# Optimization experiments

Hardware: AMD Instinct MI355X
Metric: run time of the kernel (lower is better)

## Reference

```python
import jax, jax.numpy as jnp
import numpy as np

N, E, G = 20000, 320000, 256
FXD, FXT, OD = 78, 954, 128


def _lin(key, fan_in, fan_out, scale=0.05):
    return jax.random.normal(key, (fan_in, fan_out), dtype=jnp.float32) * scale


def setup_inputs() -> dict:
    key = jax.random.key(0)
    ks = jax.random.split(key, 24)
    inp = {
        "x1": jax.random.normal(ks[0], (N, FXD), dtype=jnp.float32),
        "edge_index1": jax.random.randint(ks[1], (2, E), 0, N, dtype=jnp.int32),
        "batch1": (jnp.arange(N, dtype=jnp.int32) * G) // N,  # sorted, every graph non-empty
        "x2": jax.random.normal(ks[2], (N, FXD), dtype=jnp.float32),
        "edge_index2": jax.random.randint(ks[3], (2, E), 0, N, dtype=jnp.int32),
        "batch2": (jnp.arange(N, dtype=jnp.int32) * G) // N,
        "cell": jax.random.normal(ks[4], (G, FXT), dtype=jnp.float32),
        # GCNConv weights (shared across the two drug branches, as in the module)
        "Wc1": _lin(ks[5], FXD, FXD), "bc1": jnp.zeros((FXD,), jnp.float32),
        "Wc2": _lin(ks[6], FXD, FXD * 2), "bc2": jnp.zeros((FXD * 2,), jnp.float32),
        "Wc3": _lin(ks[7], FXD * 2, FXD * 4), "bc3": jnp.zeros((FXD * 4,), jnp.float32),
        "Wg1": _lin(ks[8], FXD * 4, FXD * 2), "bg1": jnp.zeros((FXD * 2,), jnp.float32),
        "Wg2": _lin(ks[9], FXD * 2, OD), "bg2": jnp.zeros((OD,), jnp.float32),
        # cell reduction MLP 954 -> 2048 -> 512 -> 256
        "Wr1": _lin(ks[10], FXT, 2048), "br1": jnp.zeros((2048,), jnp.float32),
        "Wr2": _lin(ks[11], 2048, 512), "br2": jnp.zeros((512,), jnp.float32),
        "Wr3": _lin(ks[12], 512, OD * 2), "br3": jnp.zeros((OD * 2,), jnp.float32),
        # head MLP 512 -> 1024 -> 512 -> 128 -> 2
        "Wf1": _lin(ks[13], OD * 4, 1024), "bf1": jnp.zeros((1024,), jnp.float32),
        "Wf2": _lin(ks[14], 1024, 512), "bf2": jnp.zeros((512,), jnp.float32),
        "Wf3": _lin(ks[15], 512, 128), "bf3": jnp.zeros((128,), jnp.float32),
        "Wo": _lin(ks[16], 128, 2), "bo": jnp.zeros((2,), jnp.float32),
    }
    return inp


def gcn_conv(x, W, b, src, dst, n):
    """PyG GCNConv: h = D^{-1/2}(A+I)D^{-1/2} (x W) + b (self-loops added)."""
    h = x @ W
    loops = jnp.arange(n, dtype=src.dtype)
    s = jnp.concatenate([src, loops])
    d = jnp.concatenate([dst, loops])
    deg = jax.ops.segment_sum(jnp.ones_like(s, dtype=h.dtype), d, num_segments=n)
    dinv = jax.lax.rsqrt(deg)  # deg >= 1 due to self-loops
    norm = dinv[s] * dinv[d]  # [E+N]
    out = jax.ops.segment_sum(h[s] * norm[:, None], d, num_segments=n)
    return out + b


def drug_branch(x, ei, batch, Wc1, bc1, Wc2, bc2, Wc3, bc3, Wg1, bg1, Wg2, bg2):
    src, dst = ei[0], ei[1]
    n = x.shape[0]
    x = jax.nn.relu(gcn_conv(x, Wc1, bc1, src, dst, n))
    x = jax.nn.relu(gcn_conv(x, Wc2, bc2, src, dst, n))
    x = jax.nn.relu(gcn_conv(x, Wc3, bc3, src, dst, n))
    x = jax.ops.segment_max(x, batch, num_segments=G)  # global max pool -> [G, 312]
    x = jax.nn.relu(x @ Wg1 + bg1)
    x = x @ Wg2 + bg2  # dropout is identity in eval mode
    return x


def reference(x1, edge_index1, batch1, x2, edge_index2, batch2, cell,
              Wc1, bc1, Wc2, bc2, Wc3, bc3, Wg1, bg1, Wg2, bg2,
              Wr1, br1, Wr2, br2, Wr3, br3,
              Wf1, bf1, Wf2, bf2, Wf3, bf3, Wo, bo):
    g1 = drug_branch(x1, edge_index1, batch1, Wc1, bc1, Wc2, bc2, Wc3, bc3, Wg1, bg1, Wg2, bg2)
    g2 = drug_branch(x2, edge_index2, batch2, Wc1, bc1, Wc2, bc2, Wc3, bc3, Wg1, bg1, Wg2, bg2)
    # F.normalize(cell, p=2, dim=1)
    cv = cell / jnp.maximum(jnp.linalg.norm(cell, axis=1, keepdims=True), 1e-12)
    cv = jax.nn.relu(cv @ Wr1 + br1)
    cv = jax.nn.relu(cv @ Wr2 + br2)
    cv = jax.nn.relu(cv @ Wr3 + br3)
    xc = jnp.concatenate([g1, g2, cv], axis=1)  # [G, 512]
    xc = jax.nn.relu(xc @ Wf1 + bf1)
    xc = jax.nn.relu(xc @ Wf2 + bf2)
    xc = jax.nn.relu(xc @ Wf3 + bf3)
    return xc @ Wo + bo  # [G, 2]
```

## Files before the change

### kernel.cpp

```cpp
#include <hip/hip_runtime.h>

#define N_NODES 20000
#define N_EDGES 320000
#define N_GRAPH 256
#define ECHUNK 2048
#define DCAP 64

__device__ __forceinline__ ushort f2b(float f) {
  unsigned u = __float_as_uint(f);
  u += 0x7FFFu + ((u >> 16) & 1u);
  return (ushort)(u >> 16);
}
__device__ __forceinline__ float b2f(ushort u) {
  return __uint_as_float(((unsigned)u) << 16);
}

typedef __attribute__((ext_vector_type(8))) short bf16x8;
typedef __attribute__((ext_vector_type(4))) float f32x4;

template <int POOL>
__launch_bounds__(256)
__global__ void gemm_mfma(const ushort* __restrict__ A, int lda,
                          const ushort* __restrict__ Bt, int ldbt,
                          void* __restrict__ Cv, int ldc,
                          const float* __restrict__ bias,
                          int Nr, int Kpad, int M, int do_relu, int obf,
                          const float* __restrict__ dsc, int cwz,
                          const int* __restrict__ bA, const int* __restrict__ bB,
                          int nsplit, int gA, int gB, int gTot) {
  constexpr int BM = 128, BN = 128, BK = 32, LK = 40;
  __shared__ __align__(16) ushort Asl[BM][LK];
  __shared__ __align__(16) ushort Bsl[BN][LK];
  const int tid = threadIdx.x;
  const int Cc = (M + BN - 1) / BN;
  const int R = (Nr + BM - 1) / BM;
  const int RR = (R + 7) >> 3;
  const int xz = blockIdx.x & 7, g = blockIdx.x >> 3;
  const int q = g / Cc;
  const int by = xz * RR + q, bx = g - q * Cc;
  if (by >= R) return;
  const int row0 = by * BM, col0 = bx * BN;

  const int lane = tid & 63, w = tid >> 6;
  const int a_r = tid >> 1, a_h = tid & 1;

  const int nst = Kpad / BK;

  uint4 pa0, pa1, pb0, pb1;
  auto load_tile = [&](int k0) {
    if (row0 + a_r < Nr) {
      const uint4* p = (const uint4*)(A + (size_t)(row0 + a_r) * lda + k0 + a_h * 16);
      pa0 = p[0]; pa1 = p[1];
    } else {
      pa0 = make_uint4(0u, 0u, 0u, 0u); pa1 = pa0;
    }
    const uint4* pq = (const uint4*)(Bt + (size_t)(col0 + a_r) * ldbt + k0 + a_h * 16);
    pb0 = pq[0]; pb1 = pq[1];
  };
  auto commit = [&]() {
    *(uint4*)&Asl[a_r][a_h * 16] = pa0;
    *(uint4*)&Asl[a_r][a_h * 16 + 8] = pa1;
    *(uint4*)&Bsl[a_r][a_h * 16] = pb0;
    *(uint4*)&Bsl[a_r][a_h * 16 + 8] = pb1;
  };

  f32x4 acc[2][8] = {};
  const int mrow = w * 32;
  const int lm = lane & 15, lq = (lane >> 4) * 8;

  load_tile(0);
  for (int t = 0; t < nst; ++t) {
    commit();
    __syncthreads();
    if (t + 1 < nst) load_tile((t + 1) * BK);
    bf16x8 af0 = *(const bf16x8*)&Asl[mrow + lm][lq];
    bf16x8 af1 = *(const bf16x8*)&Asl[mrow + 16 + lm][lq];
#pragma unroll
    for (int nt = 0; nt < 8; ++nt) {
      bf16x8 bf = *(const bf16x8*)&Bsl[nt * 16 + lm][lq];
      acc[0][nt] = __builtin_amdgcn_mfma_f32_16x16x32_bf16(af0, bf, acc[0][nt], 0, 0, 0);
      acc[1][nt] = __builtin_amdgcn_mfma_f32_16x16x32_bf16(af1, bf, acc[1][nt], 0, 0, 0);
    }
    __syncthreads();
  }

  const int rquad = (lane >> 4) * 4;

  if constexpr (POOL) {
    __shared__ int Ps[4][BN];
    for (int idx = tid; idx < 4 * BN; idx += 256) Ps[idx >> 7][idx & 127] = 0;
    __syncthreads();
    const int g0 = (row0 < nsplit) ? gA + bA[row0] : gB + bB[row0 - nsplit];
    int gr8[2][4];
#pragma unroll
    for (int mt = 0; mt < 2; ++mt)
#pragma unroll
      for (int r = 0; r < 4; ++r) {
        const int rr = row0 + mrow + mt * 16 + rquad + r;
        gr8[mt][r] = (rr < Nr)
                         ? ((rr < nsplit) ? gA + bA[rr] : gB + bB[rr - nsplit])
                         : -1;
      }
#pragma unroll
    for (int mt = 0; mt < 2; ++mt)
#pragma unroll
      for (int nt = 0; nt < 8; ++nt) {
        const int cl = nt * 16 + lm;
        if (col0 + cl >= M) continue;
        const float bv = bias[col0 + cl];
#pragma unroll
        for (int r = 0; r < 4; ++r) {
          const int gg = gr8[mt][r];
          if (gg < 0) continue;
          const float v = fmaxf(acc[mt][nt][r] + bv, 0.f);
          atomicMax(&Ps[gg - g0][cl], __float_as_int(v));
        }
      }
    __syncthreads();
    for (int idx = tid; idx < 4 * BN; idx += 256) {
      const int s = idx >> 7, c = idx & 127;
      const int gg = g0 + s, cc = col0 + c;
      if (gg < gTot && cc < M)
        atomicMax((int*)Cv + (size_t)gg * ldc + cc, Ps[s][c]);
    }
    return;
  }

  const int cz = (cwz > M) ? cwz : M;
#pragma unroll
  for (int mt = 0; mt < 2; ++mt) {
#pragma unroll
    for (int nt = 0; nt < 8; ++nt) {
      const int cc = col0 + nt * 16 + lm;
      if (cc >= cz) continue;
      const bool cval = cc < M;
      const float bv = (cval && bias) ? bias[cc] : 0.f;
#pragma unroll
      for (int r = 0; r < 4; ++r) {
        const int rr = row0 + mrow + mt * 16 + rquad + r;
        if (rr >= Nr) continue;
        float v = cval ? (acc[mt][nt][r] + bv) : 0.f;
        if (do_relu) v = fmaxf(v, 0.f);
        if (dsc) v *= dsc[rr];
        if (obf) ((ushort*)Cv)[(size_t)rr * ldc + cc] = f2b(v);
        else     ((float*)Cv)[(size_t)rr * ldc + cc] = v;
      }
    }
  }
}

struct GJob {
  const void* A; const ushort* Bt; void* C; const float* bias;
  int lda, a_f32, ldbt, ldc, Nr, Kpad, M, relu, obf, rsplit, cpad, rb, cb, blk0;
};

__launch_bounds__(256)
__global__ void gemm_grp(GJob j0, GJob j1, int njobs) {
  GJob j = (njobs > 1 && (int)blockIdx.x >= j1.blk0) ? j1 : j0;
  const int local = blockIdx.x - j.blk0;
  const int by = local / j.cb, bx = local - by * j.cb;
  const int row0 = by * 32, col0 = bx * 64;
  const int tid = threadIdx.x, lane = tid & 63, w = tid >> 6;

  __shared__ __align__(16) char smem[32768];
  ushort (*Asl)[32][40] = (ushort (*)[32][40])smem;
  ushort (*Bsl)[64][40] = (ushort (*)[64][40])(smem + 10240);
  float  (*Rs)[32][64]  = (float  (*)[32][64])smem;

  const int a_r = lane >> 1, a_h = lane & 1;
  const int lm = lane & 15, lq = (lane >> 4) * 8;
  const int nst = j.Kpad / 32;

  uint4 ra[4], rb[4];
  auto gload = [&](int t) {
    const int k0 = t * 32;
    const int ar = row0 + a_r;
    if (j.a_f32) {
      if (ar < j.Nr) {
        const uint4* p = (const uint4*)((const float*)j.A + (size_t)ar * j.lda + k0 + a_h * 16);
        ra[0] = p[0]; ra[1] = p[1]; ra[2] = p[2]; ra[3] = p[3];
      } else {
        ra[0] = make_uint4(0u, 0u, 0u, 0u); ra[1] = ra[0]; ra[2] = ra[0]; ra[3] = ra[0];
      }
    } else {
      if (ar < j.Nr) {
        const uint4* p = (const uint4*)((const ushort*)j.A + (size_t)ar * j.lda + k0 + a_h * 16);
        ra[0] = p[0]; ra[1] = p[1];
      } else {
        ra[0] = make_uint4(0u, 0u, 0u, 0u); ra[1] = ra[0];
      }
    }
    const uint4* q = (const uint4*)(j.Bt + (size_t)(col0 + lane) * j.ldbt + k0);
    rb[0] = q[0]; rb[1] = q[1]; rb[2] = q[2]; rb[3] = q[3];
  };
  auto commit = [&]() {
    if (j.a_f32) {
      ushort tmp[16];
      const float* f = (const float*)&ra[0];
#pragma unroll
      for (int q2 = 0; q2 < 16; ++q2) tmp[q2] = f2b(f[q2]);
      *(uint4*)&Asl[w][a_r][a_h * 16]     = *(uint4*)&tmp[0];
      *(uint4*)&Asl[w][a_r][a_h * 16 + 8] = *(uint4*)&tmp[8];
    } else {
      *(uint4*)&Asl[w][a_r][a_h * 16]     = ra[0];
      *(uint4*)&Asl[w][a_r][a_h * 16 + 8] = ra[1];
    }
    *(uint4*)&Bsl[w][lane][0]  = rb[0];
    *(uint4*)&Bsl[w][lane][8]  = rb[1];
    *(uint4*)&Bsl[w][lane][16] = rb[2];
    *(uint4*)&Bsl[w][lane][24] = rb[3];
  };

  f32x4 acc[2][4] = {};
  if (w < nst) {
    gload(w);
    for (int t = w; t < nst; t += 4) {
      commit();
      bf16x8 af0 = *(const bf16x8*)&Asl[w][lm][lq];
      bf16x8 af1 = *(const bf16x8*)&Asl[w][16 + lm][lq];
      bf16x8 bq0 = *(const bf16x8*)&Bsl[w][lm][lq];
      bf16x8 bq1 = *(const bf16x8*)&Bsl[w][16 + lm][lq];
      bf16x8 bq2 = *(const bf16x8*)&Bsl[w][32 + lm][lq];
      bf16x8 bq3 = *(const bf16x8*)&Bsl[w][48 + lm][lq];
      if (t + 4 < nst) gload(t + 4);
      acc[0][0] = __builtin_amdgcn_mfma_f32_16x16x32_bf16(af0, bq0, acc[0][0], 0, 0, 0);
      acc[0][1] = __builtin_amdgcn_mfma_f32_16x16x32_bf16(af0, bq1, acc[0][1], 0, 0, 0);
      acc[0][2] = __builtin_amdgcn_mfma_f32_16x16x32_bf16(af0, bq2, acc[0][2], 0, 0, 0);
      acc[0][3] = __builtin_amdgcn_mfma_f32_16x16x32_bf16(af0, bq3, acc[0][3], 0, 0, 0);
      acc[1][0] = __builtin_amdgcn_mfma_f32_16x16x32_bf16(af1, bq0, acc[1][0], 0, 0, 0);
      acc[1][1] = __builtin_amdgcn_mfma_f32_16x16x32_bf16(af1, bq1, acc[1][1], 0, 0, 0);
      acc[1][2] = __builtin_amdgcn_mfma_f32_16x16x32_bf16(af1, bq2, acc[1][2], 0, 0, 0);
      acc[1][3] = __builtin_amdgcn_mfma_f32_16x16x32_bf16(af1, bq3, acc[1][3], 0, 0, 0);
    }
  }

  __syncthreads();
  const int rquad = (lane >> 4) * 4;
#pragma unroll
  for (int mt = 0; mt < 2; ++mt)
#pragma unroll
    for (int nt = 0; nt < 4; ++nt)
#pragma unroll
      for (int r = 0; r < 4; ++r)
        Rs[w][mt * 16 + rquad + r][nt * 16 + lm] = acc[mt][nt][r];
  __syncthreads();

  const int rrow = tid >> 3, cs = (tid & 7) * 8;
  float v[8];
  {
    float4 x0 = *(const float4*)&Rs[0][rrow][cs];
    float4 x1 = *(const float4*)&Rs[0][rrow][cs + 4];
    v[0] = x0.x; v[1] = x0.y; v[2] = x0.z; v[3] = x0.w;
    v[4] = x1.x; v[5] = x1.y; v[6] = x1.z; v[7] = x1.w;
  }
#pragma unroll
  for (int ww = 1; ww < 4; ++ww) {
    float4 x0 = *(const float4*)&Rs[ww][rrow][cs];
    float4 x1 = *(const float4*)&Rs[ww][rrow][cs + 4];
    v[0] += x0.x; v[1] += x0.y; v[2] += x0.z; v[3] += x0.w;
    v[4] += x1.x; v[5] += x1.y; v[6] += x1.z; v[7] += x1.w;
  }
  const int rg = row0 + rrow;
  if (rg < j.Nr) {
    int rm = rg, rq = 0;
    if (j.rsplit) { rq = rg / j.rsplit; rm = rg - rq * j.rsplit; }
#pragma unroll
    for (int q = 0; q < 8; ++q) {
      const int cc = col0 + cs + q;
      if (cc >= j.cpad) break;
      float x = 0.f;
      if (cc < j.M) {
        x = v[q] + j.bias[cc];
        if (j.relu) x = fmaxf(x, 0.f);
      }
      const size_t di = (size_t)rm * j.ldc + (size_t)rq * j.M + cc;
      if (j.obf) ((ushort*)j.C)[di] = f2b(x);
      else       ((float*)j.C)[di] = x;
    }
  }
}

struct WJob { const float* W; ushort* T; int Mv, Kv, Mp, Kp, blk0; };
struct WArgs { WJob j[11]; int wblocks; const float* cell; ushort* cv; };

__launch_bounds__(256)
__global__ void prep_all(WArgs a) {
  const int bid = blockIdx.x, tid = threadIdx.x;
  if (bid < a.wblocks) {
    __shared__ float t[32][33];
    int ji = 0;
#pragma unroll
    for (int i = 1; i < 11; ++i)
      if (bid >= a.j[i].blk0) ji = i;
    WJob wj = a.j[ji];
    const int lt = bid - wj.blk0;
    const int ktiles = wj.Kp >> 5;
    const int tn = lt / ktiles, tk = lt - tn * ktiles;
    const int n0 = tn << 5, k0 = tk << 5;
    const int c = tid & 31, r = tid >> 5;
    const int nn = n0 + c;
#pragma unroll
    for (int i = 0; i < 4; ++i) {
      const int k = k0 + r + i * 8;
      t[r + i * 8][c] = (k < wj.Kv && nn < wj.Mv) ? wj.W[(size_t)k * wj.Mv + nn] : 0.f;
    }
    __syncthreads();
    const int k = k0 + c;
#pragma unroll
    for (int i = 0; i < 4; ++i) {
      const int n = n0 + r + i * 8;
      wj.T[(size_t)n * wj.Kp + k] = f2b(t[c][r + i * 8]);
    }
    return;
  }
  __shared__ float red[256];
  const int g = bid - a.wblocks;
  const float* row = a.cell + (size_t)g * 954;
  float s = 0.f;
  for (int f = tid; f < 954; f += 256) { float vv = row[f]; s += vv * vv; }
  red[tid] = s;
  __syncthreads();
  for (int off2 = 128; off2 > 0; off2 >>= 1) {
    if (tid < off2) red[tid] += red[tid + off2];
    __syncthreads();
  }
  const float inv = 1.f / fmaxf(sqrtf(red[0]), 1e-12f);
  ushort* orow = a.cv + (size_t)g * 960;
  for (int f = tid; f < 954; f += 256) orow[f] = f2b(row[f] * inv);
  for (int f = 954 + tid; f < 960; f += 256) orow[f] = 0;
}

template<int BM, int BN, int TM, int TN>
__launch_bounds__(256)
__global__ void gemm_t(const float* __restrict__ A, int lda,
                       const float* __restrict__ B, int ldb,
                       float* __restrict__ C, int ldc, int zstride,
                       const float* __restrict__ bias,
                       int Nr, int K, int M, int do_relu, int kchunk) {
  constexpr int BK = 16;
  constexpr int LDA = BM + 4;
  __shared__ __align__(16) float As[BK][LDA];
  __shared__ __align__(16) float Bs[BK][BN];
  const int tid = threadIdx.x;
  const int row0 = blockIdx.y * BM, col0 = blockIdx.x * BN;
  constexpr int NX = BN / TN;
  const int tx = tid % NX, ty = tid / NX;
  float acc[TM][TN] = {};
  const int klo = blockIdx.z * kchunk;
  const int khi = min(klo + kchunk, K);

  constexpr int AIT = BM * BK / 4 / 256;
  constexpr int BIT = BK * BN / 4 / 256;
  float4 pa[AIT], pb[BIT];

  auto load_tile = [&](int k0) {
#pragma unroll
    for (int it = 0; it < AIT; ++it) {
      const int s = it * 256 + tid;
      const int row = s >> 2, kq = (s & 3) << 2;
      float4 av = make_float4(0.f, 0.f, 0.f, 0.f);
      const int gr = row0 + row, gk = k0 + kq;
      if (gr < Nr) {
        const float* Ap = A + (size_t)gr * lda + gk;
        if (gk + 3 < khi) { av.x = Ap[0]; av.y = Ap[1]; av.z = Ap[2]; av.w = Ap[3]; }
        else {
          if (gk     < khi) av.x = Ap[0];
          if (gk + 1 < khi) av.y = Ap[1];
          if (gk + 2 < khi) av.z = Ap[2];
        }
      }
      pa[it] = av;
    }
#pragma unroll
    for (int it = 0; it < BIT; ++it) {
      const int s = it * 256 + tid;
      const int kr = s / (BN / 4), c = (s % (BN / 4)) << 2;
      float4 bv = make_float4(0.f, 0.f, 0.f, 0.f);
      const int gk = k0 + kr, gc = col0 + c;
      if (gk < khi) {
        const float* Bp = B + (size_t)gk * ldb + gc;
        if (gc + 3 < M) { bv.x = Bp[0]; bv.y = Bp[1]; bv.z = Bp[2]; bv.w = Bp[3]; }
        else {
          if (gc     < M) bv.x = Bp[0];
          if (gc + 1 < M) bv.y = Bp[1];
          if (gc + 2 < M) bv.z = Bp[2];
        }
      }
      pb[it] = bv;
    }
  };

  load_tile(klo);
  for (int k0 = klo; k0 < khi; k0 += BK) {
#pragma unroll
    for (int it = 0; it < AIT; ++it) {
      const int s = it * 256 + tid;
      const int row = s >> 2, kq = (s & 3) << 2;
      As[kq    ][row] = pa[it].x;
      As[kq + 1][row] = pa[it].y;
      As[kq + 2][row] = pa[it].z;
      As[kq + 3][row] = pa[it].w;
    }
#pragma unroll
    for (int it = 0; it < BIT; ++it) {
      const int s = it * 256 + tid;
      const int kr = s / (BN / 4), c = (s % (BN / 4)) << 2;
      *(float4*)&Bs[kr][c] = pb[it];
    }
    __syncthreads();
    if (k0 + BK < khi) load_tile(k0 + BK);
#pragma unroll
    for (int kk = 0; kk < BK; ++kk) {
      float ar[TM], br[TN];
#pragma unroll
      for (int i = 0; i < TM; i += 4)
        *(float4*)&ar[i] = *(const float4*)&As[kk][ty * TM + i];
      if constexpr (TN == 8) {
        *(float4*)&br[0] = *(const float4*)&Bs[kk][tx * 4];
        *(float4*)&br[4] = *(const float4*)&Bs[kk][BN / 2 + tx * 4];
      } else {
        *(float4*)&br[0] = *(const float4*)&Bs[kk][tx * TN];
      }
#pragma unroll
      for (int i = 0; i < TM; ++i)
#pragma unroll
        for (int j = 0; j < TN; ++j)
          acc[i][j] += ar[i] * br[j];
    }
    __syncthreads();
  }

  float* Cz = C + (size_t)blockIdx.z * zstride;
#pragma unroll
  for (int i = 0; i < TM; ++i) {
    const int r = row0 + ty * TM + i;
    if (r >= Nr) continue;
    float* Crow = Cz + (size_t)r * ldc;
#pragma unroll
    for (int g = 0; g < TN / 4; ++g) {
      const int c = col0 + (TN == 8 ? g * (BN / 2) : 0) + tx * 4;
      if (c + 3 < M) {
        float4 v;
        v.x = acc[i][g * 4 + 0]; v.y = acc[i][g * 4 + 1];
        v.z = acc[i][g * 4 + 2]; v.w = acc[i][g * 4 + 3];
        if (bias) { v.x += bias[c]; v.y += bias[c + 1]; v.z += bias[c + 2]; v.w += bias[c + 3]; }
        if (do_relu) {
          v.x = fmaxf(v.x, 0.f); v.y = fmaxf(v.y, 0.f);
          v.z = fmaxf(v.z, 0.f); v.w = fmaxf(v.w, 0.f);
        }
        *(float4*)&Crow[c] = v;
      } else {
#pragma unroll
        for (int j = 0; j < 4; ++j) {
          if (c + j >= M) continue;
          float v = acc[i][g * 4 + j];
          if (bias) v += bias[c + j];
          if (do_relu) v = fmaxf(v, 0.f);
          Crow[c + j] = v;
        }
      }
    }
  }
}

__global__ void scatterb_kernel(const int* __restrict__ e1, const int* __restrict__ e2,
                                int* __restrict__ cnt, ushort* __restrict__ col_idx,
                                int E, int npass, int rng) {
  const int xcd = blockIdx.x & 7;
  const int lo = xcd * rng, hi = lo + rng;
  const int base = (blockIdx.x >> 3) * ECHUNK;
  const int TE = npass * E;
  for (int i = threadIdx.x; i < ECHUNK; i += 256) {
    int e = base + i;
    if (e >= TE) break;
    int d, s;
    if (e < E) { d = e1[E + e]; s = e1[e]; }
    else { int jj = e - E; d = N_NODES + e2[E + jj]; s = N_NODES + e2[jj]; }
    if (d >= lo && d < hi) {
      int p = atomicAdd(&cnt[d], 1);
      if (p < DCAP) col_idx[((size_t)d << 6) + p] = (ushort)s;
    }
  }
}

__global__ void dinv_cvt_kernel(const int* __restrict__ cnt, float* __restrict__ dinv,
                                const float* __restrict__ xa, const float* __restrict__ xb,
                                int nsplit, ushort* __restrict__ dst, int total) {
  int gid = blockIdx.x * blockDim.x + threadIdx.x;
  if (gid >= total) return;
  int n = gid / 10, v = gid - n * 10;
  const float sc = rsqrtf((float)(cnt[n] + 1));
  if (v == 0) dinv[n] = sc;
  const float* src = (n < nsplit) ? xa + (size_t)n * 78 : xb + (size_t)(n - nsplit) * 78;
  const int f0 = v * 8;
  ushort o[8];
#pragma unroll
  for (int jj = 0; jj < 8; ++jj)
    o[jj] = (f0 + jj < 78) ? f2b(src[f0 + jj] * sc) : 0;
  ((uint4*)(dst + (size_t)n * 80))[v] = *(uint4*)o;
}

__device__ __forceinline__ void acc8(float* a, uint4 u) {
  a[0] += __uint_as_float(u.x << 16);
  a[1] += __uint_as_float(u.x & 0xFFFF0000u);
  a[2] += __uint_as_float(u.y << 16);
  a[3] += __uint_as_float(u.y & 0xFFFF0000u);
  a[4] += __uint_as_float(u.z << 16);
  a[5] += __uint_as_float(u.z & 0xFFFF0000u);
  a[6] += __uint_as_float(u.w << 16);
  a[7] += __uint_as_float(u.w & 0xFFFF0000u);
}

__global__ void aggb_flat(const ushort* __restrict__ h, const int* __restrict__ cnt,
                          const ushort* __restrict__ col_idx, const float* __restrict__ dinv,
                          ushort* __restrict__ out, int in_ld, int out_ld,
                          int V, int total) {
  int gid = blockIdx.x * blockDim.x + threadIdx.x;
  if (gid >= total) return;
  int n = gid / V, v = gid - n * V;
  const uint4* hv = (const uint4*)h;
  const int ivs = in_ld >> 3;
  float a[8] = {};
  acc8(a, hv[(size_t)n * ivs + v]);
  const int beg = n << 6;
  const int end = beg + min(cnt[n], DCAP);
  int e = beg;
  for (; e + 3 < end; e += 4) {
    int s0 = col_idx[e], s1 = col_idx[e + 1], s2 = col_idx[e + 2], s3 = col_idx[e + 3];
    uint4 u0 = hv[(size_t)s0 * ivs + v], u1 = hv[(size_t)s1 * ivs + v];
    uint4 u2 = hv[(size_t)s2 * ivs + v], u3 = hv[(size_t)s3 * ivs + v];
    acc8(a, u0); acc8(a, u1); acc8(a, u2); acc8(a, u3);
  }
  for (; e < end; ++e)
    acc8(a, hv[(size_t)col_idx[e] * ivs + v]);
  const float din = dinv[n];
  ushort o[8];
#pragma unroll
  for (int jj = 0; jj < 8; ++jj) o[jj] = f2b(din * a[jj]);
  ((uint4*)(out + (size_t)n * out_ld))[v] = *(uint4*)o;
}

extern "C" void kernel_launch(void* const* d_in, const int* in_sizes, int n_in,
                              void* d_out, int out_size, void* d_ws, size_t ws_size,
                              hipStream_t stream) {
  (void)in_sizes; (void)n_in; (void)out_size;
  const float* x1  = (const float*)d_in[0];
  const int*   ei1 = (const int*)d_in[1];
  const int*   bt1 = (const int*)d_in[2];
  const float* x2  = (const float*)d_in[3];
  const int*   ei2 = (const int*)d_in[4];
  const int*   bt2 = (const int*)d_in[5];
  const float* cell = (const float*)d_in[6];
  const float* Wc1 = (const float*)d_in[7];  const float* bc1 = (const float*)d_in[8];
  const float* Wc2 = (const float*)d_in[9];  const float* bc2 = (const float*)d_in[10];
  const float* Wc3 = (const float*)d_in[11]; const float* bc3 = (const float*)d_in[12];
  const float* Wg1 = (const float*)d_in[13]; const float* bg1 = (const float*)d_in[14];
  const float* Wg2 = (const float*)d_in[15]; const float* bg2 = (const float*)d_in[16];
  const float* Wr1 = (const float*)d_in[17]; const float* br1 = (const float*)d_in[18];
  const float* Wr2 = (const float*)d_in[19]; const float* br2 = (const float*)d_in[20];
  const float* Wr3 = (const float*)d_in[21]; const float* br3 = (const float*)d_in[22];
  const float* Wf1 = (const float*)d_in[23]; const float* bf1 = (const float*)d_in[24];
  const float* Wf2 = (const float*)d_in[25]; const float* bf2 = (const float*)d_in[26];
  const float* Wf3 = (const float*)d_in[27]; const float* bf3 = (const float*)d_in[28];
  const float* Wo  = (const float*)d_in[29]; const float* bo  = (const float*)d_in[30];
  float* out = (float*)d_out;

  const bool batched = ws_size >= (size_t)95 * 1024 * 1024;
  const int NPASS = batched ? 2 : 1;
  const int NN = NPASS * N_NODES;

  char* ws = (char*)d_ws;
  size_t off = 0;
  auto alloc_f = [&](size_t ne) {
    ne = (ne + 3) & ~(size_t)3;
    float* p = (float*)(ws + off); off += ne * 4; return p;
  };
  auto alloc_i = [&](size_t ne) {
    ne = (ne + 3) & ~(size_t)3;
    int* p = (int*)(ws + off); off += ne * 4; return p;
  };
  ushort* xb16w = (ushort*)alloc_f((size_t)NN * 80);
  ushort* ab16  = (ushort*)alloc_f((size_t)NN * 80);
  ushort* xb16s = (ushort*)alloc_f((size_t)NN * 40);
  float* dinv   = alloc_f(NN);
  int* cnt      = alloc_i(NN);
  float* pooled = alloc_f((size_t)512 * 320);
  ushort* cv16  = (ushort*)alloc_f((size_t)N_GRAPH * 480);
  ushort* wg1o  = (ushort*)alloc_f((size_t)512 * 80);
  ushort* wr1o  = (ushort*)alloc_f((size_t)256 * 1024);
  ushort* wr2o  = (ushort*)alloc_f((size_t)256 * 256);
  ushort* catbuf = (ushort*)alloc_f((size_t)256 * 256);
  ushort* wf1o  = (ushort*)alloc_f((size_t)256 * 512);
  ushort* wf2o  = (ushort*)alloc_f((size_t)256 * 256);
  float* wf3o   = alloc_f((size_t)256 * 128);
  ushort* wc1t  = (ushort*)alloc_f(128 * 96 / 2);
  ushort* wc2t  = (ushort*)alloc_f(256 * 96 / 2);
  ushort* wc3t  = (ushort*)alloc_f(384 * 160 / 2);
  ushort* wr1t  = (ushort*)alloc_f(2048 * 960 / 2);
  ushort* wr2t  = (ushort*)alloc_f(512 * 2048 / 2);
  ushort* wf1t  = (ushort*)alloc_f(1024 * 512 / 2);
  ushort* wg1t  = (ushort*)alloc_f(192 * 320 / 2);
  ushort* wg2t  = (ushort*)alloc_f(128 * 160 / 2);
  ushort* wr3t  = (ushort*)alloc_f(256 * 512 / 2);
  ushort* wf2t  = (ushort*)alloc_f(512 * 1024 / 2);
  ushort* wf3t  = (ushort*)alloc_f(128 * 512 / 2);
  ushort* col_idx = (ushort*)alloc_i((size_t)NN * DCAP / 2);

  auto gemm_small = [&](const float* A, int lda, const float* B, int ldb, float* C, int ldc,
                        const float* bias, int Nr, int K, int M, int relu) {
    dim3 grid((M + 63) / 64, (Nr + 63) / 64, 1);
    gemm_t<64, 64, 4, 4><<<grid, 256, 0, stream>>>(A, lda, B, ldb, C, ldc, 0, bias,
                                                   Nr, K, M, relu, K);
  };
  auto mfma = [&](const ushort* A, int lda, const ushort* Bt, int ldbt, void* C, int ldc,
                  const float* bias, int Nr, int Kpad, int M, int relu, int obf,
                  const float* dsc, int cwz) {
    int Cc = (M + 127) / 128, R = (Nr + 127) / 128, RR = (R + 7) >> 3;
    dim3 grid(8 * RR * Cc, 1, 1);
    gemm_mfma<0><<<grid, 256, 0, stream>>>(A, lda, Bt, ldbt, C, ldc, bias, Nr, Kpad, M,
                                           relu, obf, dsc, cwz,
                                           nullptr, nullptr, 0, 0, 0, 0);
  };
  auto mfma_pool = [&](const ushort* A, int lda, const ushort* Bt, int ldbt,
                       const float* bias, int Nr, int Kpad, int M,
                       const int* bA, const int* bB, int nsplit, int gA, int gB, int gTot) {
    int Cc = (M + 127) / 128, R = (Nr + 127) / 128, RR = (R + 7) >> 3;
    dim3 grid(8 * RR * Cc, 1, 1);
    gemm_mfma<1><<<grid, 256, 0, stream>>>(A, lda, Bt, ldbt, pooled, 320, bias,
                                           Nr, Kpad, M, 1, 0, nullptr, 0,
                                           bA, bB, nsplit, gA, gB, gTot);
  };
  auto mkjob = [&](const void* A, int lda, int a_f32, const ushort* Bt, int ldbt,
                   void* C, int ldc, const float* bias, int Nr, int Kpad, int M,
                   int relu, int obf, int rsplit, int cpad) {
    GJob g; g.A = A; g.Bt = Bt; g.C = C; g.bias = bias;
    g.lda = lda; g.a_f32 = a_f32; g.ldbt = ldbt; g.ldc = ldc;
    g.Nr = Nr; g.Kpad = Kpad; g.M = M; g.relu = relu; g.obf = obf;
    g.rsplit = rsplit; g.cpad = cpad;
    g.rb = (Nr + 31) / 32; g.cb = (M + 63) / 64; g.blk0 = 0;
    return g;
  };
  auto grp1 = [&](GJob a) {
    gemm_grp<<<a.rb * a.cb, 256, 0, stream>>>(a, a, 1);
  };
  auto grp2 = [&](GJob a, GJob b) {
    b.blk0 = a.rb * a.cb;
    gemm_grp<<<b.blk0 + b.rb * b.cb, 256, 0, stream>>>(a, b, 2);
  };

  {
    WArgs wa{};
    int nj = 0, wb = 0;
    auto addw = [&](const float* W, ushort* T, int Mv, int Kv, int Mp, int Kp) {
      wa.j[nj].W = W; wa.j[nj].T = T; wa.j[nj].Mv = Mv; wa.j[nj].Kv = Kv;
      wa.j[nj].Mp = Mp; wa.j[nj].Kp = Kp; wa.j[nj].blk0 = wb;
      wb += (Mp >> 5) * (Kp >> 5); ++nj;
    };
    addw(Wc1, wc1t,   78,   78,  128,   96);
    addw(Wc2, wc2t,  156,   78,  256,   96);
    addw(Wc3, wc3t,  312,  156,  384,  160);
    addw(Wr1, wr1t, 2048,  954, 2048,  960);
    addw(Wr2, wr2t,  512, 2048,  512, 2048);
    addw(Wf1, wf1t, 1024,  512, 1024,  512);
    addw(Wg1, wg1t,  156,  312,  192,  320);
    addw(Wg2, wg2t,  128,  156,  128,  160);
    addw(Wr3, wr3t,  256,  512,  256,  512);
    addw(Wf2, wf2t,  512, 1024,  512, 1024);
    addw(Wf3, wf3t,  128,  512,  128,  512);
    wa.wblocks = wb; wa.cell = cell; wa.cv = cv16;
    prep_all<<<wb + N_GRAPH, 256, 0, stream>>>(wa);
  }

  auto drug_pass = [&](const float* xa, const float* xb, const int* eia, const int* eib,
                       const int* bta, const int* btb, int npass, int pool_base,
                       int zero_pool) {
    const int nn = npass * N_NODES;
    const int te = npass * N_EDGES;
    const int rng = nn / 8;
    const int echunks = (te + ECHUNK - 1) / ECHUNK;
    hipMemsetAsync(cnt, 0, (size_t)nn * 4 + (zero_pool ? (size_t)512 * 320 * 4 : 0),
                   stream);
    scatterb_kernel<<<8 * echunks, 256, 0, stream>>>(eia, eib, cnt, col_idx,
                                                     N_EDGES, npass, rng);
    {
      int tot = nn * 10;
      dinv_cvt_kernel<<<(tot + 255) / 256, 256, 0, stream>>>(
          cnt, dinv, xa, xb, (npass == 2) ? N_NODES : nn, xb16s, tot);
    }
    {
      int tot = nn * 10;
      aggb_flat<<<(tot + 255) / 256, 256, 0, stream>>>(xb16s, cnt, col_idx, dinv,
                                                       ab16, 80, 96, 10, tot);
    }
    mfma(ab16, 96, wc1t, 96, xb16s, 80, bc1, nn, 96, 78, 1, 1, dinv, 80);
    {
      int tot = nn * 10;
      aggb_flat<<<(tot + 255) / 256, 256, 0, stream>>>(xb16s, cnt, col_idx, dinv,
                                                       ab16, 80, 96, 10, tot);
    }
    mfma(ab16, 96, wc2t, 96, xb16w, 160, bc2, nn, 96, 156, 1, 1, dinv, 160);
    {
      int tot = nn * 20;
      aggb_flat<<<(tot + 255) / 256, 256, 0, stream>>>(xb16w, cnt, col_idx, dinv,
                                                       ab16, 160, 160, 20, tot);
    }
    mfma_pool(ab16, 160, wc3t, 160, bc3, nn, 160, 312,
              bta, btb, (npass == 2) ? N_NODES : nn,
              pool_base, pool_base + N_GRAPH, pool_base + npass * N_GRAPH);
  };

  if (batched) {
    drug_pass(x1, x2, ei1, ei2, bt1, bt2, 2, 0, 1);
  } else {
    drug_pass(x1, x1, ei1, ei1, bt1, bt1, 1, 0, 1);
    drug_pass(x2, x2, ei2, ei2, bt2, bt2, 1, N_GRAPH, 0);
  }

  grp2(mkjob(pooled, 320, 1, wg1t, 320, wg1o, 160, bg1, 512, 320, 156, 1, 1, 0, 160),
       mkjob(cv16,   960, 0, wr1t, 960, wr1o, 2048, br1, 256, 960, 2048, 1, 1, 0, 2048));
  grp2(mkjob(wg1o,  160, 0, wg2t,  160, catbuf, 512, bg2, 512,  160,  128, 0, 1, 256, 128),
       mkjob(wr1o, 2048, 0, wr2t, 2048, wr2o,   512, br2, 256, 2048,  512, 1, 1, 0, 512));
  grp1(mkjob(wr2o, 512, 0, wr3t, 512, catbuf + 256, 512, br3, 256, 512, 256, 1, 1, 0, 256));
  grp1(mkjob(catbuf, 512, 0, wf1t,  512, wf1o, 1024, bf1, 256,  512, 1024, 1, 1, 0, 1024));
  grp1(mkjob(wf1o,  1024, 0, wf2t, 1024, wf2o,  512, bf2, 256, 1024,  512, 1, 1, 0, 512));
  grp1(mkjob(wf2o,   512, 0, wf3t,  512, wf3o,  128, bf3, 256,  512,  128, 1, 0, 0, 128));
  gemm_small(wf3o, 128, Wo, 2, out, 2, bo, N_GRAPH, 128, 2, 0);
}
```

Measured before the change: 398.6 us.

## Fuse GCN aggregation into MFMA GEMM and merge edge scatter into prep kernel

Adds a gemm_fused kernel that performs the neighbour aggregation for layers 1 and 2 straight into shared memory and then runs the bf16 MFMA GEMM with bias, ReLU and dinv scaling. This removes two separate aggregation kernels and the round-trip of the aggregated matrix through global memory. The edge scatter is folded into the prep_all launch in the batched path, and the final 128x2 GEMM becomes a tiny dedicated kernel, all to cut launch count. In exchange, the fused kernel redoes the gather per 64-row tile, has lower MFMA tile occupancy, and adds a non-batched path with separate memsets.

```diff
diff --git a/kernel.cpp b/kernel.cpp
--- a/kernel.cpp
+++ b/kernel.cpp
@@ -17,6 +17,107 @@
 
 typedef __attribute__((ext_vector_type(8))) short bf16x8;
 typedef __attribute__((ext_vector_type(4))) float f32x4;
+
+__device__ __forceinline__ void acc8(float* a, uint4 u) {
+  a[0] += __uint_as_float(u.x << 16);
+  a[1] += __uint_as_float(u.x & 0xFFFF0000u);
+  a[2] += __uint_as_float(u.y << 16);
+  a[3] += __uint_as_float(u.y & 0xFFFF0000u);
+  a[4] += __uint_as_float(u.z << 16);
+  a[5] += __uint_as_float(u.z & 0xFFFF0000u);
+  a[6] += __uint_as_float(u.w << 16);
+  a[7] += __uint_as_float(u.w & 0xFFFF0000u);
+}
+
+template <int BN_T>
+__launch_bounds__(256)
+__global__ void gemm_fused(const ushort* __restrict__ h,
+                           const int* __restrict__ cnt,
+                           const ushort* __restrict__ col_idx,
+                           const float* __restrict__ dinv,
+                           const ushort* __restrict__ Bt, int ldbt,
+                           ushort* __restrict__ C, int ldc,
+                           const float* __restrict__ bias,
+                           int Nr, int M, int cwz) {
+  constexpr int BM = 64, BN = BN_T * 16, LA = 104;
+  __shared__ __align__(16) ushort Afull[BM][LA];
+  __shared__ __align__(16) ushort Bsl[BN][40];
+  const int tid = threadIdx.x;
+  const int R = (Nr + BM - 1) / BM;
+  const int RR = (R + 7) >> 3;
+  const int xz = blockIdx.x & 7, g = blockIdx.x >> 3;
+  const int by = xz * RR + g;
+  if (by >= R) return;
+  const int row0 = by * BM;
+  const int lane = tid & 63, w = tid >> 6;
+  const uint4* hv = (const uint4*)h;
+
+  for (int task = tid; task < BM * 10; task += 256) {
+    const int r = task / 10, c = task - r * 10;
+    const int n = row0 + r;
+    uint4 val = make_uint4(0u, 0u, 0u, 0u);
+    if (n < Nr) {
+      float a[8] = {};
+      acc8(a, hv[(size_t)n * 10 + c]);
+      const int beg = n << 6;
+      const int end = beg + min(cnt[n], DCAP);
+      int e = beg;
+      for (; e + 3 < end; e += 4) {
+        int s0 = col_idx[e], s1 = col_idx[e + 1];
+        int s2 = col_idx[e + 2], s3 = col_idx[e + 3];
+        acc8(a, hv[(size_t)s0 * 10 + c]); acc8(a, hv[(size_t)s1 * 10 + c]);
+        acc8(a, hv[(size_t)s2 * 10 + c]); acc8(a, hv[(size_t)s3 * 10 + c]);
+      }
+      for (; e < end; ++e) acc8(a, hv[(size_t)col_idx[e] * 10 + c]);
+      const float dn = dinv[n];
+      ushort o[8];
+#pragma unroll
+      for (int j = 0; j < 8; ++j) o[j] = f2b(dn * a[j]);
+      val = *(uint4*)o;
+    }
+    *(uint4*)&Afull[r][c * 8] = val;
+  }
+  for (int task = tid; task < BM * 2; task += 256) {
+    const int r = task >> 1, c2 = task & 1;
+    *(uint4*)&Afull[r][80 + c2 * 8] = make_uint4(0u, 0u, 0u, 0u);
+  }
+  __syncthreads();
+
+  f32x4 acc[BN_T] = {};
+  const int mrow = w * 16;
+  const int lm = lane & 15, lq = (lane >> 4) * 8;
+  for (int t = 0; t < 3; ++t) {
+    const int k0 = t * 32;
+    for (int s = tid; s < BN * 4; s += 256) {
+      const int br = s >> 2, bo = (s & 3) * 8;
+      *(uint4*)&Bsl[br][bo] = *(const uint4*)&Bt[(size_t)br * ldbt + k0 + bo];
+    }
+    __syncthreads();
+    bf16x8 af = *(const bf16x8*)&Afull[mrow + lm][k0 + lq];
+#pragma unroll
+    for (int nt = 0; nt < BN_T; ++nt) {
+      bf16x8 bf = *(const bf16x8*)&Bsl[nt * 16 + lm][lq];
+      acc[nt] = __builtin_amdgcn_mfma_f32_16x16x32_bf16(af, bf, acc[nt], 0, 0, 0);
+    }
+    __syncthreads();
+  }
+
+  const int rquad = (lane >> 4) * 4;
+#pragma unroll
+  for (int nt = 0; nt < BN_T; ++nt) {
+    const int cc = nt * 16 + lm;
+    if (cc >= cwz) continue;
+    const bool cval = cc < M;
+    const float bv = cval ? bias[cc] : 0.f;
+#pragma unroll
+    for (int r = 0; r < 4; ++r) {
+      const int rr = row0 + mrow + rquad + r;
+      if (rr >= Nr) continue;
+      float v = cval ? fmaxf(acc[nt][r] + bv, 0.f) * dinv[rr] : 0.f;
+      C[(size_t)rr * ldc + cc] = f2b(v);
+    }
+  }
+}
 
 template <int POOL>
 __launch_bounds__(256)
@@ -281,7 +382,10 @@
 }
 
 struct WJob { const float* W; ushort* T; int Mv, Kv, Mp, Kp, blk0; };
-struct WArgs { WJob j[11]; int wblocks; const float* cell; ushort* cv; };
+struct WArgs {
+  WJob j[11]; int wblocks; const float* cell; ushort* cv;
+  const int* e1; const int* e2; int* cnt; ushort* col; int E, npass, rng, scatB;
+};
 
 __launch_bounds__(256)
 __global__ void prep_all(WArgs a) {
@@ -313,152 +417,38 @@
     }
     return;
   }
-  __shared__ float red[256];
-  const int g = bid - a.wblocks;
-  const float* row = a.cell + (size_t)g * 954;
-  float s = 0.f;
-  for (int f = tid; f < 954; f += 256) { float vv = row[f]; s += vv * vv; }
-  red[tid] = s;
-  __syncthreads();
-  for (int off2 = 128; off2 > 0; off2 >>= 1) {
-    if (tid < off2) red[tid] += red[tid + off2];
+  if (bid < a.wblocks + N_GRAPH) {
+    __shared__ float red[256];
+    const int g = bid - a.wblocks;
+    const float* row = a.cell + (size_t)g * 954;
+    float s = 0.f;
+    for (int f = tid; f < 954; f += 256) { float vv = row[f]; s += vv * vv; }
+    red[tid] = s;
     __syncthreads();
-  }
-  const float inv = 1.f / fmaxf(sqrtf(red[0]), 1e-12f);
-  ushort* orow = a.cv + (size_t)g * 960;
-  for (int f = tid; f < 954; f += 256) orow[f] = f2b(row[f] * inv);
-  for (int f = 954 + tid; f < 960; f += 256) orow[f] = 0;
-}
-
-template<int BM, int BN, int TM, int TN>
-__launch_bounds__(256)
-__global__ void gemm_t(const float* __restrict__ A, int lda,
-                       const float* __restrict__ B, int ldb,
-                       float* __restrict__ C, int ldc, int zstride,
-                       const float* __restrict__ bias,
-                       int Nr, int K, int M, int do_relu, int kchunk) {
-  constexpr int BK = 16;
-  constexpr int LDA = BM + 4;
-  __shared__ __align__(16) float As[BK][LDA];
-  __shared__ __align__(16) float Bs[BK][BN];
-  const int tid = threadIdx.x;
-  const int row0 = blockIdx.y * BM, col0 = blockIdx.x * BN;
-  constexpr int NX = BN / TN;
-  const int tx = tid % NX, ty = tid / NX;
-  float acc[TM][TN] = {};
-  const int klo = blockIdx.z * kchunk;
-  const int khi = min(klo + kchunk, K);
-
-  constexpr int AIT = BM * BK / 4 / 256;
-  constexpr int BIT = BK * BN / 4 / 256;
-  float4 pa[AIT], pb[BIT];
-
-  auto load_tile = [&](int k0) {
-#pragma unroll
-    for (int it = 0; it < AIT; ++it) {
-      const int s = it * 256 + tid;
-      const int row = s >> 2, kq = (s & 3) << 2;
-      float4 av = make_float4(0.f, 0.f, 0.f, 0.f);
-      const int gr = row0 + row, gk = k0 + kq;
-      if (gr < Nr) {
-        const float* Ap = A + (size_t)gr * lda + gk;
-        if (gk + 3 < khi) { av.x = Ap[0]; av.y = Ap[1]; av.z = Ap[2]; av.w = Ap[3]; }
-        else {
-          if (gk     < khi) av.x = Ap[0];
-          if (gk + 1 < khi) av.y = Ap[1];
-          if (gk + 2 < khi) av.z = Ap[2];
-        }
-      }
-      pa[it] = av;
-    }
-#pragma unroll
-    for (int it = 0; it < BIT; ++it) {
-      const int s = it * 256 + tid;
-      const int kr = s / (BN / 4), c = (s % (BN / 4)) << 2;
-      float4 bv = make_float4(0.f, 0.f, 0.f, 0.f);
-      const int gk = k0 + kr, gc = col0 + c;
-      if (gk < khi) {
-        const float* Bp = B + (size_t)gk * ldb + gc;
-        if (gc + 3 < M) { bv.x = Bp[0]; bv.y = Bp[1]; bv.z = Bp[2]; bv.w = Bp[3]; }
-        else {
-          if (gc     < M) bv.x = Bp[0];
-          if (gc + 1 < M) bv.y = Bp[1];
-          if (gc + 2 < M) bv.z = Bp[2];
-        }
-      }
-      pb[it] = bv;
-    }
-  };
-
-  load_tile(klo);
-  for (int k0 = klo; k0 < khi; k0 += BK) {
-#pragma unroll
-    for (int it = 0; it < AIT; ++it) {
-      const int s = it * 256 + tid;
-      const int row = s >> 2, kq = (s & 3) << 2;
-      As[kq    ][row] = pa[it].x;
-      As[kq + 1][row] = pa[it].y;
-      As[kq + 2][row] = pa[it].z;
-      As[kq + 3][row] = pa[it].w;
-    }
-#pragma unroll
-    for (int it = 0; it < BIT; ++it) {
-      const int s = it * 256 + tid;
-      const int kr = s / (BN / 4), c = (s % (BN / 4)) << 2;
-      *(float4*)&Bs[kr][c] = pb[it];
-    }
-    __syncthreads();
-    if (k0 + BK < khi) load_tile(k0 + BK);
-#pragma unroll
-    for (int kk = 0; kk < BK; ++kk) {
-      float ar[TM], br[TN];
-#pragma unroll
-      for (int i = 0; i < TM; i += 4)
-        *(float4*)&ar[i] = *(const float4*)&As[kk][ty * TM + i];
-      if constexpr (TN == 8) {
-        *(float4*)&br[0] = *(const float4*)&Bs[kk][tx * 4];
-        *(float4*)&br[4] = *(const float4*)&Bs[kk][BN / 2 + tx * 4];
-      } else {
-        *(float4*)&br[0] = *(const float4*)&Bs[kk][tx * TN];
-      }
-#pragma unroll
-      for (int i = 0; i < TM; ++i)
-#pragma unroll
-        for (int j = 0; j < TN; ++j)
-          acc[i][j] += ar[i] * br[j];
-    }
-    __syncthreads();
-  }
-
-  float* Cz = C + (size_t)blockIdx.z * zstride;
-#pragma unroll
-  for (int i = 0; i < TM; ++i) {
-    const int r = row0 + ty * TM + i;
-    if (r >= Nr) continue;
-    float* Crow = Cz + (size_t)r * ldc;
-#pragma unroll
-    for (int g = 0; g < TN / 4; ++g) {
-      const int c = col0 + (TN == 8 ? g * (BN / 2) : 0) + tx * 4;
-      if (c + 3 < M) {
-        float4 v;
-        v.x = acc[i][g * 4 + 0]; v.y = acc[i][g * 4 + 1];
-        v.z = acc[i][g * 4 + 2]; v.w = acc[i][g * 4 + 3];
-        if (bias) { v.x += bias[c]; v.y += bias[c + 1]; v.z += bias[c + 2]; v.w += bias[c + 3]; }
-        if (do_relu) {
-          v.x = fmaxf(v.x, 0.f); v.y = fmaxf(v.y, 0.f);
-          v.z = fmaxf(v.z, 0.f); v.w = fmaxf(v.w, 0.f);
-        }
-        *(float4*)&Crow[c] = v;
-      } else {
-#pragma unroll
-        for (int j = 0; j < 4; ++j) {
-          if (c + j >= M) continue;
-          float v = acc[i][g * 4 + j];
-          if (bias) v += bias[c + j];
-          if (do_relu) v = fmaxf(v, 0.f);
-          Crow[c + j] = v;
-        }
-      }
+    for (int off2 = 128; off2 > 0; off2 >>= 1) {
+      if (tid < off2) red[tid] += red[tid + off2];
+      __syncthreads();
+    }
+    const float inv = 1.f / fmaxf(sqrtf(red[0]), 1e-12f);
+    ushort* orow = a.cv + (size_t)g * 960;
+    for (int f = tid; f < 954; f += 256) orow[f] = f2b(row[f] * inv);
+    for (int f = 954 + tid; f < 960; f += 256) orow[f] = 0;
+    return;
+  }
+  const int sb = bid - a.wblocks - N_GRAPH;
+  const int xcd = sb & 7;
+  const int lo = xcd * a.rng, hi = lo + a.rng;
+  const int base = (sb >> 3) * ECHUNK;
+  const int TE = a.npass * a.E;
+  for (int i = tid; i < ECHUNK; i += 256) {
+    int e = base + i;
+    if (e >= TE) break;
+    int d, s;
+    if (e < a.E) { d = a.e1[a.E + e]; s = a.e1[e]; }
+    else { int jj = e - a.E; d = N_NODES + a.e2[a.E + jj]; s = N_NODES + a.e2[jj]; }
+    if (d >= lo && d < hi) {
+      int p = atomicAdd(&a.cnt[d], 1);
+      if (p < DCAP) a.col[((size_t)d << 6) + p] = (ushort)s;
     }
   }
 }
@@ -498,17 +488,6 @@
   for (int jj = 0; jj < 8; ++jj)
     o[jj] = (f0 + jj < 78) ? f2b(src[f0 + jj] * sc) : 0;
   ((uint4*)(dst + (size_t)n * 80))[v] = *(uint4*)o;
-}
-
-__device__ __forceinline__ void acc8(float* a, uint4 u) {
-  a[0] += __uint_as_float(u.x << 16);
-  a[1] += __uint_as_float(u.x & 0xFFFF0000u);
-  a[2] += __uint_as_float(u.y << 16);
-  a[3] += __uint_as_float(u.y & 0xFFFF0000u);
-  a[4] += __uint_as_float(u.z << 16);
-  a[5] += __uint_as_float(u.z & 0xFFFF0000u);
-  a[6] += __uint_as_float(u.w << 16);
-  a[7] += __uint_as_float(u.w & 0xFFFF0000u);
 }
 
 __global__ void aggb_flat(const ushort* __restrict__ h, const int* __restrict__ cnt,
@@ -538,6 +517,17 @@
 #pragma unroll
   for (int jj = 0; jj < 8; ++jj) o[jj] = f2b(din * a[jj]);
   ((uint4*)(out + (size_t)n * out_ld))[v] = *(uint4*)o;
+}
+
+__global__ void wo_kernel(const float* __restrict__ wf3o, const float* __restrict__ Wo,
+                          const float* __restrict__ bo, float* __restrict__ out) {
+  int gid = blockIdx.x * blockDim.x + threadIdx.x;
+  if (gid >= N_GRAPH * 2) return;
+  int row = gid >> 1, col = gid & 1;
+  float v = bo[col];
+  const float* a = wf3o + (size_t)row * 128;
+  for (int k = 0; k < 128; ++k) v += a[k] * Wo[k * 2 + col];
+  out[gid] = v;
 }
 
 extern "C" void kernel_launch(void* const* d_in, const int* in_sizes, int n_in,
@@ -594,7 +584,7 @@
   ushort* wf2o  = (ushort*)alloc_f((size_t)256 * 256);
   float* wf3o   = alloc_f((size_t)256 * 128);
   ushort* wc1t  = (ushort*)alloc_f(128 * 96 / 2);
-  ushort* wc2t  = (ushort*)alloc_f(256 * 96 / 2);
+  ushort* wc2t  = (ushort*)alloc_f(192 * 96 / 2);
   ushort* wc3t  = (ushort*)alloc_f(384 * 160 / 2);
   ushort* wr1t  = (ushort*)alloc_f(2048 * 960 / 2);
   ushort* wr2t  = (ushort*)alloc_f(512 * 2048 / 2);
@@ -606,21 +596,6 @@
   ushort* wf3t  = (ushort*)alloc_f(128 * 512 / 2);
   ushort* col_idx = (ushort*)alloc_i((size_t)NN * DCAP / 2);
 
-  auto gemm_small = [&](const float* A, int lda, const float* B, int ldb, float* C, int ldc,
-                        const float* bias, int Nr, int K, int M, int relu) {
-    dim3 grid((M + 63) / 64, (Nr + 63) / 64, 1);
-    gemm_t<64, 64, 4, 4><<<grid, 256, 0, stream>>>(A, lda, B, ldb, C, ldc, 0, bias,
-                                                   Nr, K, M, relu, K);
-  };
-  auto mfma = [&](const ushort* A, int lda, const ushort* Bt, int ldbt, void* C, int ldc,
-                  const float* bias, int Nr, int Kpad, int M, int relu, int obf,
-                  const float* dsc, int cwz) {
-    int Cc = (M + 127) / 128, R = (Nr + 127) / 128, RR = (R + 7) >> 3;
-    dim3 grid(8 * RR * Cc, 1, 1);
-    gemm_mfma<0><<<grid, 256, 0, stream>>>(A, lda, Bt, ldbt, C, ldc, bias, Nr, Kpad, M,
-                                           relu, obf, dsc, cwz,
-                                           nullptr, nullptr, 0, 0, 0, 0);
-  };
   auto mfma_pool = [&](const ushort* A, int lda, const ushort* Bt, int ldbt,
                        const float* bias, int Nr, int Kpad, int M,
                        const int* bA, const int* bB, int nsplit, int gA, int gB, int gTot) {
@@ -648,16 +623,17 @@
     gemm_grp<<<b.blk0 + b.rb * b.cb, 256, 0, stream>>>(a, b, 2);
   };
 
+  WArgs wa{};
+  int wb = 0;
   {
-    WArgs wa{};
-    int nj = 0, wb = 0;
+    int nj = 0;
     auto addw = [&](const float* W, ushort* T, int Mv, int Kv, int Mp, int Kp) {
       wa.j[nj].W = W; wa.j[nj].T = T; wa.j[nj].Mv = Mv; wa.j[nj].Kv = Kv;
       wa.j[nj].Mp = Mp; wa.j[nj].Kp = Kp; wa.j[nj].blk0 = wb;
       wb += (Mp >> 5) * (Kp >> 5); ++nj;
     };
     addw(Wc1, wc1t,   78,   78,  128,   96);
-    addw(Wc2, wc2t,  156,   78,  256,   96);
+    addw(Wc2, wc2t,  156,   78,  192,   96);
     addw(Wc3, wc3t,  312,  156,  384,  160);
     addw(Wr1, wr1t, 2048,  954, 2048,  960);
     addw(Wr2, wr2t,  512, 2048,  512, 2048);
@@ -668,52 +644,52 @@
     addw(Wf2, wf2t,  512, 1024,  512, 1024);
     addw(Wf3, wf3t,  128,  512,  128,  512);
     wa.wblocks = wb; wa.cell = cell; wa.cv = cv16;
-    prep_all<<<wb + N_GRAPH, 256, 0, stream>>>(wa);
-  }
-
-  auto drug_pass = [&](const float* xa, const float* xb, const int* eia, const int* eib,
-                       const int* bta, const int* btb, int npass, int pool_base,
-                       int zero_pool) {
+  }
+
+  auto node_layers = [&](const float* xa, const float* xb,
+                         const int* bta, const int* btb, int npass, int pool_base) {
     const int nn = npass * N_NODES;
-    const int te = npass * N_EDGES;
-    const int rng = nn / 8;
-    const int echunks = (te + ECHUNK - 1) / ECHUNK;
-    hipMemsetAsync(cnt, 0, (size_t)nn * 4 + (zero_pool ? (size_t)512 * 320 * 4 : 0),
-                   stream);
-    scatterb_kernel<<<8 * echunks, 256, 0, stream>>>(eia, eib, cnt, col_idx,
-                                                     N_EDGES, npass, rng);
     {
       int tot = nn * 10;
       dinv_cvt_kernel<<<(tot + 255) / 256, 256, 0, stream>>>(
           cnt, dinv, xa, xb, (npass == 2) ? N_NODES : nn, xb16s, tot);
     }
-    {
-      int tot = nn * 10;
-      aggb_flat<<<(tot + 255) / 256, 256, 0, stream>>>(xb16s, cnt, col_idx, dinv,
-                                                       ab16, 80, 96, 10, tot);
-    }
-    mfma(ab16, 96, wc1t, 96, xb16s, 80, bc1, nn, 96, 78, 1, 1, dinv, 80);
-    {
-      int tot = nn * 10;
-      aggb_flat<<<(tot + 255) / 256, 256, 0, stream>>>(xb16s, cnt, col_idx, dinv,
-                                                       ab16, 80, 96, 10, tot);
-    }
-    mfma(ab16, 96, wc2t, 96, xb16w, 160, bc2, nn, 96, 156, 1, 1, dinv, 160);
+    const int R = (nn + 63) / 64, RR = (R + 7) >> 3;
+    dim3 fgrid(8 * RR, 1, 1);
+    gemm_fused<8><<<fgrid, 256, 0, stream>>>(xb16s, cnt, col_idx, dinv, wc1t, 96,
+                                             (ushort*)ab16, 80, bc1, nn, 78, 80);
+    gemm_fused<12><<<fgrid, 256, 0, stream>>>((ushort*)ab16, cnt, col_idx, dinv, wc2t, 96,
+                                              xb16w, 160, bc2, nn, 156, 160);
     {
       int tot = nn * 20;
       aggb_flat<<<(tot + 255) / 256, 256, 0, stream>>>(xb16w, cnt, col_idx, dinv,
-                                                       ab16, 160, 160, 20, tot);
-    }
-    mfma_pool(ab16, 160, wc3t, 160, bc3, nn, 160, 312,
+                                                       (ushort*)ab16, 160, 160, 20, tot);
+    }
+    mfma_pool((ushort*)ab16, 160, wc3t, 160, bc3, nn, 160, 312,
               bta, btb, (npass == 2) ? N_NODES : nn,
               pool_base, pool_base + N_GRAPH, pool_base + npass * N_GRAPH);
   };
 
   if (batched) {
-    drug_pass(x1, x2, ei1, ei2, bt1, bt2, 2, 0, 1);
+    const int echunks = (2 * N_EDGES + ECHUNK - 1) / ECHUNK;
+    hipMemsetAsync(cnt, 0, (size_t)NN * 4 + (size_t)512 * 320 * 4, stream);
+    wa.e1 = ei1; wa.e2 = ei2; wa.cnt = cnt; wa.col = col_idx;
+    wa.E = N_EDGES; wa.npass = 2; wa.rng = NN / 8; wa.scatB = 8 * echunks;
+    prep_all<<<wb + N_GRAPH + wa.scatB, 256, 0, stream>>>(wa);
+    node_layers(x1, x2, bt1, bt2, 2, 0);
   } else {
-    drug_pass(x1, x1, ei1, ei1, bt1, bt1, 1, 0, 1);
-    drug_pass(x2, x2, ei2, ei2, bt2, bt2, 1, N_GRAPH, 0);
+    wa.e1 = ei1; wa.e2 = ei1; wa.cnt = cnt; wa.col = col_idx;
+    wa.E = N_EDGES; wa.npass = 1; wa.rng = N_NODES / 8; wa.scatB = 0;
+    prep_all<<<wb + N_GRAPH, 256, 0, stream>>>(wa);
+    const int echunks = (N_EDGES + ECHUNK - 1) / ECHUNK;
+    hipMemsetAsync(cnt, 0, (size_t)N_NODES * 4 + (size_t)512 * 320 * 4, stream);
+    scatterb_kernel<<<8 * echunks, 256, 0, stream>>>(ei1, ei1, cnt, col_idx,
+                                                     N_EDGES, 1, N_NODES / 8);
+    node_layers(x1, x1, bt1, bt1, 1, 0);
+    hipMemsetAsync(cnt, 0, (size_t)N_NODES * 4, stream);
+    scatterb_kernel<<<8 * echunks, 256, 0, stream>>>(ei2, ei2, cnt, col_idx,
+                                                     N_EDGES, 1, N_NODES / 8);
+    node_layers(x2, x2, bt2, bt2, 1, N_GRAPH);
   }
 
   grp2(mkjob(pooled, 320, 1, wg1t, 320, wg1o, 160, bg1, 512, 320, 156, 1, 1, 0, 160),
@@ -724,5 +700,5 @@
   grp1(mkjob(catbuf, 512, 0, wf1t,  512, wf1o, 1024, bf1, 256,  512, 1024, 1, 1, 0, 1024));
   grp1(mkjob(wf1o,  1024, 0, wf2t, 1024, wf2o,  512, bf2, 256, 1024,  512, 1, 1, 0, 512));
   grp1(mkjob(wf2o,   512, 0, wf3t,  512, wf3o,  128, bf3, 256,  512,  128, 1, 0, 0, 128));
-  gemm_small(wf3o, 128, Wo, 2, out, 2, bo, N_GRAPH, 128, 2, 0);
-}
+  wo_kernel<<<2, 256, 0, stream>>>(wf3o, Wo, bo, out);
+}
```

Result: faster. 368.6 us (-7.5%).
